# Kernel optimization log

Measured on AMD Instinct MI355X. Metric: run time of the kernel, lower is better.

## Reference

```python
import jax, jax.numpy as jnp
import numpy as np

N_NODES = 100000
N_EDGES = 600000
D_IN = 128
D_HID = 128


def gcn_conv(x, W, b, src, dst, n_nodes):
    # PyG GCNConv: add self-loops, symmetric deg^-1/2 normalization,
    # linear transform, scatter-add aggregation, bias.
    xw = x @ W  # [N, H]
    self_loop = jnp.arange(n_nodes, dtype=src.dtype)
    s = jnp.concatenate([src, self_loop])  # sources j
    d = jnp.concatenate([dst, self_loop])  # targets i
    deg = jax.ops.segment_sum(jnp.ones_like(d, dtype=xw.dtype), d,
                              num_segments=n_nodes)
    dinv = jnp.where(deg > 0, jax.lax.rsqrt(deg), 0.0)
    norm = dinv[s] * dinv[d]  # [E+N]
    msg = xw[s] * norm[:, None]  # gather + scale
    out = jax.ops.segment_sum(msg, d, num_segments=n_nodes)
    return out + b


def setup_inputs() -> dict:
    key = jax.random.key(0)
    ks = jax.random.split(key, 4)
    x = jax.random.normal(ks[0], (N_NODES, D_IN), dtype=jnp.float32)
    edge_index = jax.random.randint(ks[1], (2, N_EDGES), 0, N_NODES,
                                    dtype=jnp.int32)
    W1 = jax.random.normal(ks[2], (D_IN, D_HID), dtype=jnp.float32) / np.sqrt(D_IN)
    b1 = jnp.zeros((D_HID,), dtype=jnp.float32)
    W2 = jax.random.normal(ks[3], (D_HID, D_HID), dtype=jnp.float32) / np.sqrt(D_HID)
    b2 = jnp.zeros((D_HID,), dtype=jnp.float32)
    return {"x": x, "edge_index": edge_index, "W1": W1, "b1": b1,
            "W2": W2, "b2": b2}


def reference(x, edge_index, W1, b1, W2, b2):
    src, dst = edge_index[0], edge_index[1]
    n = x.shape[0]
    z = gcn_conv(x, W1, b1, src, dst, n)
    z = jax.nn.relu(z)
    z = gcn_conv(z, W2, b2, src, dst, n)
    # decode: per-edge dot product of endpoint embeddings
    return jnp.sum(z[src] * z[dst], axis=1)  # [E]
```

## Files before the change

kernel.cpp:

```cpp
#include <hip/hip_runtime.h>


typedef __attribute__((ext_vector_type(8))) short short8;
typedef __attribute__((ext_vector_type(4))) float f32x4;

__device__ __forceinline__ unsigned bf16_rne(float x) {
  unsigned u = __builtin_bit_cast(unsigned, x);
  return (u + 0x7FFFu + ((u >> 16) & 1u)) >> 16;
}
__device__ __forceinline__ float bf2f(unsigned short u) {
  return __builtin_bit_cast(float, ((unsigned)u) << 16);
}

__global__ __launch_bounds__(256) void deg_kernel(const int* __restrict__ dst,
                                                  int* __restrict__ deg, int E) {
  int base = blockIdx.x * 1024 + threadIdx.x;
#pragma unroll
  for (int i = 0; i < 4; ++i) {
    int e = base + i * 256;
    if (e < E) atomicAdd(&deg[dst[e]], 1);
  }
}

__global__ __launch_bounds__(512) void scan1_kernel(const int* __restrict__ in,
                                                    int* __restrict__ tmp,
                                                    int* __restrict__ bsums, int n) {
  __shared__ int sm[2][512];
  int t = threadIdx.x;
  int gid = blockIdx.x * 512 + t;
  int v = (gid < n) ? in[gid] : 0;
  int pp = 0;
  sm[0][t] = v;
  __syncthreads();
  for (int off = 1; off < 512; off <<= 1) {
    int nv = sm[pp][t];
    if (t >= off) nv += sm[pp][t - off];
    sm[pp ^ 1][t] = nv;
    pp ^= 1;
    __syncthreads();
  }
  int inc = sm[pp][t];
  if (gid < n) tmp[gid] = inc;
  if (t == 511) bsums[blockIdx.x] = inc;
}

__global__ __launch_bounds__(256) void scan2_kernel(int* bsums, int nb) {
  __shared__ int sm[2][256];
  int t = threadIdx.x;
  int v = (t < nb) ? bsums[t] : 0;
  int pp = 0;
  sm[0][t] = v;
  __syncthreads();
  for (int off = 1; off < 256; off <<= 1) {
    int nv = sm[pp][t];
    if (t >= off) nv += sm[pp][t - off];
    sm[pp ^ 1][t] = nv;
    pp ^= 1;
    __syncthreads();
  }
  int inc = sm[pp][t];
  if (t < nb) bsums[t] = inc - v;
}

__global__ __launch_bounds__(256) void scan3_kernel(const int* __restrict__ tmp,
                                                    const int* __restrict__ bsums,
                                                    const int* __restrict__ deg,
                                                    int* __restrict__ rowptr,
                                                    float* __restrict__ dinv, int n) {
  int gid = blockIdx.x * 256 + threadIdx.x;
  if (gid < n) {
    rowptr[gid + 1] = tmp[gid] + bsums[gid >> 9];
    dinv[gid] = rsqrtf((float)(deg[gid] + 1));
  }
  if (gid == 0) rowptr[0] = 0;
}

__global__ __launch_bounds__(256) void scatter_kernel(const int* __restrict__ src,
                                                      const int* __restrict__ dst,
                                                      const int* __restrict__ rowptr,
                                                      int* __restrict__ cnt,
                                                      int2* __restrict__ csr, int E) {
  int base = blockIdx.x * 1024 + threadIdx.x;
#pragma unroll
  for (int i = 0; i < 4; ++i) {
    int e = base + i * 256;
    if (e < E) {
      int d = dst[e];
      int pos = rowptr[d] + atomicAdd(&cnt[d], 1);
      csr[pos] = make_int2(src[e], e);
    }
  }
}

__global__ __launch_bounds__(256) void wpack_kernel(const float* __restrict__ W,
                                                    short* __restrict__ Wp) {
  int t = blockIdx.x * 256 + threadIdx.x;
  if (t >= 2048) return;
  int lane = t & 63;
  int kf = (t >> 6) & 3;
  int ct = t >> 8;
  int col = ct * 16 + (lane & 15);
  int k0 = kf * 32 + (lane >> 4) * 8;
  short* dh = Wp + ((((0 * 8 + ct) * 4 + kf) * 64) + lane) * 8;
  short* dl = Wp + ((((1 * 8 + ct) * 4 + kf) * 64) + lane) * 8;
  for (int j = 0; j < 8; ++j) {
    float w = W[(k0 + j) * 128 + col];
    unsigned h = bf16_rne(w);
    float hf = __builtin_bit_cast(float, h << 16);
    unsigned lo = bf16_rne(w - hf);
    dh[j] = (short)h;
    dl[j] = (short)lo;
  }
}

__global__ __launch_bounds__(256, 4) void gemm1_kernel(const float* __restrict__ A,
                                                       const short* __restrict__ Wp,
                                                       const float* __restrict__ dinv,
                                                       unsigned short* __restrict__ out,
                                                       int M) {
  __shared__ short8 lds_a[256];

  const int tid = threadIdx.x;
  const int wave = tid >> 6;
  const int lane = tid & 63;
  const int quad = lane >> 4;
  const int l15 = lane & 15;
  const int ct0 = wave * 2;
  const int ct1 = wave * 2 + 1;
  const int colbase = wave * 32 + l15;
  const int rb0 = blockIdx.x * 16;
  const bool full = (rb0 + 16 <= M);
  const short8* Wp8 = (const short8*)Wp;

  {
    const int row = tid >> 4;
    const int seg = tid & 15;
    float4 a0 = {0.f, 0.f, 0.f, 0.f}, a1 = {0.f, 0.f, 0.f, 0.f};
    if (full || rb0 + row < M) {
      const float4* p = (const float4*)A + (size_t)(rb0 + row) * 32 + seg * 2;
      a0 = p[0];
      a1 = p[1];
    }
    const float av[8] = {a0.x, a0.y, a0.z, a0.w, a1.x, a1.y, a1.z, a1.w};
    short8 w;
#pragma unroll
    for (int j = 0; j < 8; ++j) w[j] = (short)bf16_rne(av[j]);
    lds_a[row * 16 + (seg ^ (row & 7))] = w;
  }

  short8 bh0[4], bh1[4], bl0[4], bl1[4];
#pragma unroll
  for (int f = 0; f < 4; ++f) {
    bh0[f] = Wp8[((0 * 8 + ct0) * 4 + f) * 64 + lane];
    bh1[f] = Wp8[((0 * 8 + ct1) * 4 + f) * 64 + lane];
    bl0[f] = Wp8[((1 * 8 + ct0) * 4 + f) * 64 + lane];
    bl1[f] = Wp8[((1 * 8 + ct1) * 4 + f) * 64 + lane];
  }

  __syncthreads();

  short8 af[4];
#pragma unroll
  for (int f = 0; f < 4; ++f) af[f] = lds_a[l15 * 16 + ((f * 4 + quad) ^ (l15 & 7))];

  f32x4 a0h = {0.f, 0.f, 0.f, 0.f};
  f32x4 a0l = {0.f, 0.f, 0.f, 0.f};
  f32x4 a1h = {0.f, 0.f, 0.f, 0.f};
  f32x4 a1l = {0.f, 0.f, 0.f, 0.f};
#pragma unroll
  for (int f = 0; f < 4; ++f) {
    a0h = __builtin_amdgcn_mfma_f32_16x16x32_bf16(af[f], bh0[f], a0h, 0, 0, 0);
    a1h = __builtin_amdgcn_mfma_f32_16x16x32_bf16(af[f], bh1[f], a1h, 0, 0, 0);
    a0l = __builtin_amdgcn_mfma_f32_16x16x32_bf16(af[f], bl0[f], a0l, 0, 0, 0);
    a1l = __builtin_amdgcn_mfma_f32_16x16x32_bf16(af[f], bl1[f], a1l, 0, 0, 0);
  }

  if (full) {
    const f32x4 dv = *(const f32x4*)(dinv + rb0 + quad * 4);
#pragma unroll
    for (int i = 0; i < 4; ++i) {
      const int r = rb0 + quad * 4 + i;
      out[(size_t)r * 128 + colbase] =
          (unsigned short)bf16_rne((a0h[i] + a0l[i]) * dv[i]);
      out[(size_t)r * 128 + colbase + 16] =
          (unsigned short)bf16_rne((a1h[i] + a1l[i]) * dv[i]);
    }
  } else {
#pragma unroll
    for (int i = 0; i < 4; ++i) {
      const int r = rb0 + quad * 4 + i;
      if (r < M) {
        const float d = dinv[r];
        out[(size_t)r * 128 + colbase] =
            (unsigned short)bf16_rne((a0h[i] + a0l[i]) * d);
        out[(size_t)r * 128 + colbase + 16] =
            (unsigned short)bf16_rne((a1h[i] + a1l[i]) * d);
      }
    }
  }
}

__global__ __launch_bounds__(256) void agg_gemm_kernel(
    const unsigned short* __restrict__ xw, const float* __restrict__ dinv,
    const int* __restrict__ rowptr, const int2* __restrict__ csr,
    const float* __restrict__ bias, const short* __restrict__ Wp,
    unsigned short* __restrict__ out, int N) {
  __shared__ short8 z1t[16][16];

  const int tid = threadIdx.x;
  const int node0 = blockIdx.x * 16;
  const int n = tid >> 4;
  const int l = tid & 15;
  const int node = node0 + n;

  short8 o = {0, 0, 0, 0, 0, 0, 0, 0};
  if (node < N) {
    const short8* xw8 = (const short8*)xw;
    short8 sv = xw8[(size_t)node * 16 + l];
    float acc[8];
#pragma unroll
    for (int j = 0; j < 8; ++j) acc[j] = bf2f((unsigned short)sv[j]);
    int s = rowptr[node], e = rowptr[node + 1];
    int k = s;
    for (; k + 4 <= e; k += 4) {
      int j0 = csr[k].x, j1 = csr[k + 1].x, j2 = csr[k + 2].x, j3 = csr[k + 3].x;
      short8 v0 = xw8[(size_t)j0 * 16 + l];
      short8 v1 = xw8[(size_t)j1 * 16 + l];
      short8 v2 = xw8[(size_t)j2 * 16 + l];
      short8 v3 = xw8[(size_t)j3 * 16 + l];
#pragma unroll
      for (int j = 0; j < 8; ++j) {
        acc[j] += (bf2f((unsigned short)v0[j]) + bf2f((unsigned short)v1[j])) +
                  (bf2f((unsigned short)v2[j]) + bf2f((unsigned short)v3[j]));
      }
    }
    for (; k < e; ++k) {
      short8 v = xw8[(size_t)csr[k].x * 16 + l];
#pragma unroll
      for (int j = 0; j < 8; ++j) acc[j] += bf2f((unsigned short)v[j]);
    }
    float di = dinv[node];
    const float4* b4 = (const float4*)bias;
    float4 bb0 = b4[l * 2], bb1 = b4[l * 2 + 1];
    float bv[8] = {bb0.x, bb0.y, bb0.z, bb0.w, bb1.x, bb1.y, bb1.z, bb1.w};
#pragma unroll
    for (int j = 0; j < 8; ++j) {
      float v = fmaf(di, acc[j], bv[j]);
      v = fmaxf(v, 0.f);
      o[j] = (short)bf16_rne(v);
    }
  }
  z1t[n][l ^ n] = o;
  __syncthreads();

  const int wave = tid >> 6;
  const int lane = tid & 63;
  const int quad = lane >> 4;
  const int l15 = lane & 15;
  const int ct0 = wave * 2;
  const int ct1 = wave * 2 + 1;

  short8 af[4];
#pragma unroll
  for (int f = 0; f < 4; ++f) af[f] = z1t[l15][(f * 4 + quad) ^ l15];

  const short8* Wp8 = (const short8*)Wp;
  f32x4 a0h = {0.f, 0.f, 0.f, 0.f};
  f32x4 a0l = {0.f, 0.f, 0.f, 0.f};
  f32x4 a1h = {0.f, 0.f, 0.f, 0.f};
  f32x4 a1l = {0.f, 0.f, 0.f, 0.f};
#pragma unroll
  for (int f = 0; f < 4; ++f) {
    const short8 bh0 = Wp8[((0 * 8 + ct0) * 4 + f) * 64 + lane];
    const short8 bh1 = Wp8[((0 * 8 + ct1) * 4 + f) * 64 + lane];
    const short8 bl0 = Wp8[((1 * 8 + ct0) * 4 + f) * 64 + lane];
    const short8 bl1 = Wp8[((1 * 8 + ct1) * 4 + f) * 64 + lane];
    a0h = __builtin_amdgcn_mfma_f32_16x16x32_bf16(af[f], bh0, a0h, 0, 0, 0);
    a1h = __builtin_amdgcn_mfma_f32_16x16x32_bf16(af[f], bh1, a1h, 0, 0, 0);
    a0l = __builtin_amdgcn_mfma_f32_16x16x32_bf16(af[f], bl0, a0l, 0, 0, 0);
    a1l = __builtin_amdgcn_mfma_f32_16x16x32_bf16(af[f], bl1, a1l, 0, 0, 0);
  }

  if (node0 + 16 <= N) {
    const f32x4 dv = *(const f32x4*)(dinv + node0 + quad * 4);
#pragma unroll
    for (int i = 0; i < 4; ++i) {
      const int r = node0 + quad * 4 + i;
      out[(size_t)r * 128 + ct0 * 16 + l15] =
          (unsigned short)bf16_rne((a0h[i] + a0l[i]) * dv[i]);
      out[(size_t)r * 128 + ct1 * 16 + l15] =
          (unsigned short)bf16_rne((a1h[i] + a1l[i]) * dv[i]);
    }
  } else {
#pragma unroll
    for (int i = 0; i < 4; ++i) {
      const int r = node0 + quad * 4 + i;
      if (r < N) {
        const float d = dinv[r];
        out[(size_t)r * 128 + ct0 * 16 + l15] =
            (unsigned short)bf16_rne((a0h[i] + a0l[i]) * d);
        out[(size_t)r * 128 + ct1 * 16 + l15] =
            (unsigned short)bf16_rne((a1h[i] + a1l[i]) * d);
      }
    }
  }
}

__global__ __launch_bounds__(256) void agg_kernel(const unsigned short* __restrict__ xw,
                                                  const float* __restrict__ dinv,
                                                  const int* __restrict__ rowptr,
                                                  const int2* __restrict__ csr,
                                                  const float* __restrict__ bias,
                                                  unsigned short* __restrict__ out,
                                                  int relu, int N) {
  int node = blockIdx.x * 16 + (threadIdx.x >> 4);
  int l = threadIdx.x & 15;
  if (node >= N) return;
  const short8* xw8 = (const short8*)xw;
  short8 sv = xw8[(size_t)node * 16 + l];
  float acc[8];
#pragma unroll
  for (int j = 0; j < 8; ++j) acc[j] = bf2f((unsigned short)sv[j]);
  int s = rowptr[node], e = rowptr[node + 1];
  int k = s;
  for (; k + 4 <= e; k += 4) {
    int j0 = csr[k].x, j1 = csr[k + 1].x, j2 = csr[k + 2].x, j3 = csr[k + 3].x;
    short8 v0 = xw8[(size_t)j0 * 16 + l];
    short8 v1 = xw8[(size_t)j1 * 16 + l];
    short8 v2 = xw8[(size_t)j2 * 16 + l];
    short8 v3 = xw8[(size_t)j3 * 16 + l];
#pragma unroll
    for (int j = 0; j < 8; ++j) {
      acc[j] += (bf2f((unsigned short)v0[j]) + bf2f((unsigned short)v1[j])) +
                (bf2f((unsigned short)v2[j]) + bf2f((unsigned short)v3[j]));
    }
  }
  for (; k < e; ++k) {
    short8 v = xw8[(size_t)csr[k].x * 16 + l];
#pragma unroll
    for (int j = 0; j < 8; ++j) acc[j] += bf2f((unsigned short)v[j]);
  }
  float di = dinv[node];
  const float4* b4 = (const float4*)bias;
  float4 bb0 = b4[l * 2], bb1 = b4[l * 2 + 1];
  float bv[8] = {bb0.x, bb0.y, bb0.z, bb0.w, bb1.x, bb1.y, bb1.z, bb1.w};
  short8 o;
#pragma unroll
  for (int j = 0; j < 8; ++j) {
    float v = fmaf(di, acc[j], bv[j]);
    if (relu) v = fmaxf(v, 0.f);
    o[j] = (short)bf16_rne(v);
  }
  ((short8*)out)[(size_t)node * 16 + l] = o;
}

__global__ __launch_bounds__(256) void decode_kernel(const unsigned short* __restrict__ z,
                                                     const int* __restrict__ rowptr,
                                                     const int2* __restrict__ csr,
                                                     float* __restrict__ out, int N) {
  int node = blockIdx.x * 16 + (threadIdx.x >> 4);
  int l = threadIdx.x & 15;
  if (node >= N) return;
  const short8* z8 = (const short8*)z;
  short8 zv = z8[(size_t)node * 16 + l];
  float zd[8];
#pragma unroll
  for (int j = 0; j < 8; ++j) zd[j] = bf2f((unsigned short)zv[j]);
  int s = rowptr[node], e = rowptr[node + 1];
  int k = s;
  for (; k + 4 <= e; k += 4) {
    int2 c0 = csr[k], c1 = csr[k + 1], c2 = csr[k + 2], c3 = csr[k + 3];
    short8 v0 = z8[(size_t)c0.x * 16 + l];
    short8 v1 = z8[(size_t)c1.x * 16 + l];
    short8 v2 = z8[(size_t)c2.x * 16 + l];
    short8 v3 = z8[(size_t)c3.x * 16 + l];
    float p0 = 0.f, p1 = 0.f, p2 = 0.f, p3 = 0.f;
#pragma unroll
    for (int j = 0; j < 8; ++j) {
      p0 = fmaf(zd[j], bf2f((unsigned short)v0[j]), p0);
      p1 = fmaf(zd[j], bf2f((unsigned short)v1[j]), p1);
      p2 = fmaf(zd[j], bf2f((unsigned short)v2[j]), p2);
      p3 = fmaf(zd[j], bf2f((unsigned short)v3[j]), p3);
    }
#pragma unroll
    for (int off = 8; off > 0; off >>= 1) {
      p0 += __shfl_xor(p0, off);
      p1 += __shfl_xor(p1, off);
      p2 += __shfl_xor(p2, off);
      p3 += __shfl_xor(p3, off);
    }
    if (l == 0) {
      out[c0.y] = p0;
      out[c1.y] = p1;
      out[c2.y] = p2;
      out[c3.y] = p3;
    }
  }
  for (; k < e; ++k) {
    int2 c = csr[k];
    short8 v = z8[(size_t)c.x * 16 + l];
    float p = 0.f;
#pragma unroll
    for (int j = 0; j < 8; ++j) p = fmaf(zd[j], bf2f((unsigned short)v[j]), p);
#pragma unroll
    for (int off = 8; off > 0; off >>= 1) p += __shfl_xor(p, off);
    if (l == 0) out[c.y] = p;
  }
}

extern "C" void kernel_launch(void* const* d_in, const int* in_sizes, int n_in,
                              void* d_out, int out_size, void* d_ws, size_t ws_size,
                              hipStream_t stream) {
  const float* x  = (const float*)d_in[0];
  const int*   ei = (const int*)d_in[1];
  const float* W1 = (const float*)d_in[2];
  const float* b1 = (const float*)d_in[3];
  const float* W2 = (const float*)d_in[4];
  const float* b2 = (const float*)d_in[5];

  const int N = in_sizes[0] / 128;
  const int E = in_sizes[1] / 2;
  const int* src = ei;
  const int* dst = ei + E;

  char* ws = (char*)d_ws;
  size_t off = 0;
  auto alloc = [&](size_t bytes) -> void* {
    void* p = ws + off;
    off += (bytes + 255) & ~(size_t)255;
    return p;
  };
  unsigned short* bufA = (unsigned short*)alloc((size_t)N * 128 * 2);
  unsigned short* bufB = (unsigned short*)alloc((size_t)N * 128 * 2);
  float* dinv    = (float*)alloc((size_t)N * 4);
  int*   rowptr  = (int*)alloc((size_t)(N + 1) * 4);
  int2*  csr     = (int2*)alloc((size_t)E * 8);
  short* Wp1     = (short*)alloc((size_t)2 * 8 * 4 * 64 * 8 * 2);
  short* Wp2     = (short*)alloc((size_t)2 * 8 * 4 * 64 * 8 * 2);
  int*   tmp     = (int*)alloc((size_t)N * 4);
  int*   deg     = (int*)alloc((size_t)N * 4);
  int*   cnt     = (int*)alloc((size_t)N * 4);
  int*   bsums   = (int*)alloc(1024);
  size_t zbytes = ((char*)bsums + 1024) - (char*)deg;
  hipMemsetAsync(deg, 0, zbytes, stream);

  const int E4B = (E + 1023) / 1024;
  const int NB = (N + 255) / 256;
  const int SB = (N + 511) / 512;

  wpack_kernel<<<8, 256, 0, stream>>>(W1, Wp1);
  wpack_kernel<<<8, 256, 0, stream>>>(W2, Wp2);

  deg_kernel<<<E4B, 256, 0, stream>>>(dst, deg, E);
  scan1_kernel<<<SB, 512, 0, stream>>>(deg, tmp, bsums, N);
  scan2_kernel<<<1, 256, 0, stream>>>(bsums, SB);
  scan3_kernel<<<NB, 256, 0, stream>>>(tmp, bsums, deg, rowptr, dinv, N);
  scatter_kernel<<<E4B, 256, 0, stream>>>(src, dst, rowptr, cnt, csr, E);

  const int G16 = (N + 15) / 16;
  const int AB = (N + 15) / 16;
  const int DB = (N + 15) / 16;

  gemm1_kernel<<<G16, 256, 0, stream>>>(x, Wp1, dinv, bufA, N);
  agg_gemm_kernel<<<AB, 256, 0, stream>>>(bufA, dinv, rowptr, csr, b1, Wp2,
                                          bufB, N);
  agg_kernel<<<AB, 256, 0, stream>>>(bufB, dinv, rowptr, csr, b2, bufA, 0, N);
  decode_kernel<<<DB, 256, 0, stream>>>(bufA, rowptr, csr, (float*)d_out, N);
}
```

Measured before the change: 292.8 us.

## Merge setup kernels to cut launches and shrink agg/decode block size

Folds the two weight-pack kernels and the degree count into one prep kernel. Merges scan2 and scan3 so every block redoes the small block-sum scan itself, and runs the CSR scatter in the same launch as the first GEMM, split by block index. Agg and decode now use 128-thread blocks with 8 nodes each. The goal is to remove launch gaps and improve tail balance. The risk is that scatter and gemm now share one launch, so gemm blocks may run alongside the scatter atomics and compete for bandwidth.

```diff
diff --git a/kernel.cpp b/kernel.cpp
--- a/kernel.cpp
+++ b/kernel.cpp
@@ -12,13 +12,43 @@
   return __builtin_bit_cast(float, ((unsigned)u) << 16);
 }
 
-__global__ __launch_bounds__(256) void deg_kernel(const int* __restrict__ dst,
-                                                  int* __restrict__ deg, int E) {
-  int base = blockIdx.x * 1024 + threadIdx.x;
-#pragma unroll
-  for (int i = 0; i < 4; ++i) {
-    int e = base + i * 256;
-    if (e < E) atomicAdd(&deg[dst[e]], 1);
+__device__ __forceinline__ void wpack_body(const float* __restrict__ W,
+                                           short* __restrict__ Wp, int t) {
+  int lane = t & 63;
+  int kf = (t >> 6) & 3;
+  int ct = t >> 8;
+  int col = ct * 16 + (lane & 15);
+  int k0 = kf * 32 + (lane >> 4) * 8;
+  short* dh = Wp + ((((0 * 8 + ct) * 4 + kf) * 64) + lane) * 8;
+  short* dl = Wp + ((((1 * 8 + ct) * 4 + kf) * 64) + lane) * 8;
+  for (int j = 0; j < 8; ++j) {
+    float w = W[(k0 + j) * 128 + col];
+    unsigned h = bf16_rne(w);
+    float hf = __builtin_bit_cast(float, h << 16);
+    unsigned lo = bf16_rne(w - hf);
+    dh[j] = (short)h;
+    dl[j] = (short)lo;
+  }
+}
+
+__global__ __launch_bounds__(256) void prep_kernel(const float* __restrict__ W1,
+                                                   short* __restrict__ Wp1,
+                                                   const float* __restrict__ W2,
+                                                   short* __restrict__ Wp2,
+                                                   const int* __restrict__ dst,
+                                                   int* __restrict__ deg, int E) {
+  const int b = blockIdx.x;
+  if (b < 8) {
+    wpack_body(W1, Wp1, b * 256 + threadIdx.x);
+  } else if (b < 16) {
+    wpack_body(W2, Wp2, (b - 8) * 256 + threadIdx.x);
+  } else {
+    int base = (b - 16) * 1024 + threadIdx.x;
+#pragma unroll
+    for (int i = 0; i < 4; ++i) {
+      int e = base + i * 256;
+      if (e < E) atomicAdd(&deg[dst[e]], 1);
+    }
   }
 }
 
@@ -44,10 +74,17 @@
   if (t == 511) bsums[blockIdx.x] = inc;
 }
 
-__global__ __launch_bounds__(256) void scan2_kernel(int* bsums, int nb) {
+__global__ __launch_bounds__(256) void scan23_kernel(const int* __restrict__ tmp,
+                                                     const int* __restrict__ bsums,
+                                                     const int* __restrict__ deg,
+                                                     int* __restrict__ rowptr,
+                                                     float* __restrict__ dinv,
+                                                     int n, int nb) {
   __shared__ int sm[2][256];
+  __shared__ int orig[256];
   int t = threadIdx.x;
   int v = (t < nb) ? bsums[t] : 0;
+  orig[t] = v;
   int pp = 0;
   sm[0][t] = v;
   __syncthreads();
@@ -58,68 +95,38 @@
     pp ^= 1;
     __syncthreads();
   }
-  int inc = sm[pp][t];
-  if (t < nb) bsums[t] = inc - v;
-}
-
-__global__ __launch_bounds__(256) void scan3_kernel(const int* __restrict__ tmp,
-                                                    const int* __restrict__ bsums,
-                                                    const int* __restrict__ deg,
-                                                    int* __restrict__ rowptr,
-                                                    float* __restrict__ dinv, int n) {
-  int gid = blockIdx.x * 256 + threadIdx.x;
+  int gid = blockIdx.x * 256 + t;
   if (gid < n) {
-    rowptr[gid + 1] = tmp[gid] + bsums[gid >> 9];
+    int b = gid >> 9;
+    rowptr[gid + 1] = tmp[gid] + (sm[pp][b] - orig[b]);
     dinv[gid] = rsqrtf((float)(deg[gid] + 1));
   }
   if (gid == 0) rowptr[0] = 0;
 }
 
-__global__ __launch_bounds__(256) void scatter_kernel(const int* __restrict__ src,
-                                                      const int* __restrict__ dst,
-                                                      const int* __restrict__ rowptr,
-                                                      int* __restrict__ cnt,
-                                                      int2* __restrict__ csr, int E) {
-  int base = blockIdx.x * 1024 + threadIdx.x;
-#pragma unroll
-  for (int i = 0; i < 4; ++i) {
-    int e = base + i * 256;
-    if (e < E) {
-      int d = dst[e];
-      int pos = rowptr[d] + atomicAdd(&cnt[d], 1);
-      csr[pos] = make_int2(src[e], e);
-    }
-  }
-}
-
-__global__ __launch_bounds__(256) void wpack_kernel(const float* __restrict__ W,
-                                                    short* __restrict__ Wp) {
-  int t = blockIdx.x * 256 + threadIdx.x;
-  if (t >= 2048) return;
-  int lane = t & 63;
-  int kf = (t >> 6) & 3;
-  int ct = t >> 8;
-  int col = ct * 16 + (lane & 15);
-  int k0 = kf * 32 + (lane >> 4) * 8;
-  short* dh = Wp + ((((0 * 8 + ct) * 4 + kf) * 64) + lane) * 8;
-  short* dl = Wp + ((((1 * 8 + ct) * 4 + kf) * 64) + lane) * 8;
-  for (int j = 0; j < 8; ++j) {
-    float w = W[(k0 + j) * 128 + col];
-    unsigned h = bf16_rne(w);
-    float hf = __builtin_bit_cast(float, h << 16);
-    unsigned lo = bf16_rne(w - hf);
-    dh[j] = (short)h;
-    dl[j] = (short)lo;
-  }
-}
-
-__global__ __launch_bounds__(256, 4) void gemm1_kernel(const float* __restrict__ A,
-                                                       const short* __restrict__ Wp,
-                                                       const float* __restrict__ dinv,
-                                                       unsigned short* __restrict__ out,
-                                                       int M) {
+__global__ __launch_bounds__(256, 4) void scatgemm_kernel(
+    const int* __restrict__ src, const int* __restrict__ dst,
+    const int* __restrict__ rowptr, int* __restrict__ cnt,
+    int2* __restrict__ csr, int E, int SCB, const float* __restrict__ A,
+    const short* __restrict__ Wp, const float* __restrict__ dinv,
+    unsigned short* __restrict__ out, int M) {
   __shared__ short8 lds_a[256];
 
+  if ((int)blockIdx.x < SCB) {
+    int base = blockIdx.x * 1024 + threadIdx.x;
+#pragma unroll
+    for (int i = 0; i < 4; ++i) {
+      int e = base + i * 256;
+      if (e < E) {
+        int d = dst[e];
+        int pos = rowptr[d] + atomicAdd(&cnt[d], 1);
+        csr[pos] = make_int2(src[e], e);
+      }
+    }
+    return;
+  }
+
+  const int bid = blockIdx.x - SCB;
   const int tid = threadIdx.x;
   const int wave = tid >> 6;
   const int lane = tid & 63;
@@ -128,7 +135,7 @@
   const int ct0 = wave * 2;
   const int ct1 = wave * 2 + 1;
   const int colbase = wave * 32 + l15;
-  const int rb0 = blockIdx.x * 16;
+  const int rb0 = bid * 16;
   const bool full = (rb0 + 16 <= M);
   const short8* Wp8 = (const short8*)Wp;
 
@@ -306,14 +313,14 @@
   }
 }
 
-__global__ __launch_bounds__(256) void agg_kernel(const unsigned short* __restrict__ xw,
+__global__ __launch_bounds__(128) void agg_kernel(const unsigned short* __restrict__ xw,
                                                   const float* __restrict__ dinv,
                                                   const int* __restrict__ rowptr,
                                                   const int2* __restrict__ csr,
                                                   const float* __restrict__ bias,
                                                   unsigned short* __restrict__ out,
                                                   int relu, int N) {
-  int node = blockIdx.x * 16 + (threadIdx.x >> 4);
+  int node = blockIdx.x * 8 + (threadIdx.x >> 4);
   int l = threadIdx.x & 15;
   if (node >= N) return;
   const short8* xw8 = (const short8*)xw;
@@ -354,11 +361,11 @@
   ((short8*)out)[(size_t)node * 16 + l] = o;
 }
 
-__global__ __launch_bounds__(256) void decode_kernel(const unsigned short* __restrict__ z,
+__global__ __launch_bounds__(128) void decode_kernel(const unsigned short* __restrict__ z,
                                                      const int* __restrict__ rowptr,
                                                      const int2* __restrict__ csr,
                                                      float* __restrict__ out, int N) {
-  int node = blockIdx.x * 16 + (threadIdx.x >> 4);
+  int node = blockIdx.x * 8 + (threadIdx.x >> 4);
   int l = threadIdx.x & 15;
   if (node >= N) return;
   const short8* z8 = (const short8*)z;
@@ -447,23 +454,17 @@
   const int E4B = (E + 1023) / 1024;
   const int NB = (N + 255) / 256;
   const int SB = (N + 511) / 512;
-
-  wpack_kernel<<<8, 256, 0, stream>>>(W1, Wp1);
-  wpack_kernel<<<8, 256, 0, stream>>>(W2, Wp2);
-
-  deg_kernel<<<E4B, 256, 0, stream>>>(dst, deg, E);
+  const int G16 = (N + 15) / 16;
+  const int AB16 = (N + 15) / 16;
+  const int AB8 = (N + 7) / 8;
+
+  prep_kernel<<<16 + E4B, 256, 0, stream>>>(W1, Wp1, W2, Wp2, dst, deg, E);
   scan1_kernel<<<SB, 512, 0, stream>>>(deg, tmp, bsums, N);
-  scan2_kernel<<<1, 256, 0, stream>>>(bsums, SB);
-  scan3_kernel<<<NB, 256, 0, stream>>>(tmp, bsums, deg, rowptr, dinv, N);
-  scatter_kernel<<<E4B, 256, 0, stream>>>(src, dst, rowptr, cnt, csr, E);
-
-  const int G16 = (N + 15) / 16;
-  const int AB = (N + 15) / 16;
-  const int DB = (N + 15) / 16;
-
-  gemm1_kernel<<<G16, 256, 0, stream>>>(x, Wp1, dinv, bufA, N);
-  agg_gemm_kernel<<<AB, 256, 0, stream>>>(bufA, dinv, rowptr, csr, b1, Wp2,
-                                          bufB, N);
-  agg_kernel<<<AB, 256, 0, stream>>>(bufB, dinv, rowptr, csr, b2, bufA, 0, N);
-  decode_kernel<<<DB, 256, 0, stream>>>(bufA, rowptr, csr, (float*)d_out, N);
-}
+  scan23_kernel<<<NB, 256, 0, stream>>>(tmp, bsums, deg, rowptr, dinv, N, SB);
+  scatgemm_kernel<<<E4B + G16, 256, 0, stream>>>(src, dst, rowptr, cnt, csr, E,
+                                                 E4B, x, Wp1, dinv, bufA, N);
+  agg_gemm_kernel<<<AB16, 256, 0, stream>>>(bufA, dinv, rowptr, csr, b1, Wp2,
+                                            bufB, N);
+  agg_kernel<<<AB8, 128, 0, stream>>>(bufB, dinv, rowptr, csr, b2, bufA, 0, N);
+  decode_kernel<<<AB8, 128, 0, stream>>>(bufA, rowptr, csr, (float*)d_out, N);
+}
```

Result: faster. 282.6 us (-3.5%).
